# Kernel optimization log

Measured on AMD Instinct MI355X. Metric: run time of the kernel, lower is better.

## Reference

```python
import jax, jax.numpy as jnp
import numpy as np

N_NODES = 50000


def _sage_max(x, src, dst, W_l, b_l, W_r):
    # gather neighbor (source) features, scatter-max to destination nodes
    msgs = x[src]                                   # [E, F]
    agg = jax.ops.segment_max(msgs, dst, num_segments=N_NODES)  # [N, F], -inf for empty
    agg = jnp.where(jnp.isneginf(agg), 0.0, agg)    # PyG fills isolated nodes with 0
    return agg @ W_l + b_l + x @ W_r                # lin_l(aggr) + lin_r(x)


def setup_inputs() -> dict:
    key = jax.random.key(0)
    ks = jax.random.split(key, 9)
    F_IN, H, OUT, E, EL = 128, 256, 32, 800000, 200000
    x = jax.random.normal(ks[0], (N_NODES, F_IN), dtype=jnp.float32)
    edge_index = jax.random.randint(ks[1], (2, E), 0, N_NODES, dtype=jnp.int64)
    edge_label_index = jax.random.randint(ks[2], (2, EL), 0, N_NODES, dtype=jnp.int64)
    s1 = 1.0 / np.sqrt(F_IN)
    s2 = 1.0 / np.sqrt(H)
    W1_l = jax.random.normal(ks[3], (F_IN, H), dtype=jnp.float32) * s1
    b1 = jnp.zeros((H,), dtype=jnp.float32)
    W1_r = jax.random.normal(ks[4], (F_IN, H), dtype=jnp.float32) * s1
    W2_l = jax.random.normal(ks[5], (H, OUT), dtype=jnp.float32) * s2
    b2 = jnp.zeros((OUT,), dtype=jnp.float32)
    W2_r = jax.random.normal(ks[6], (H, OUT), dtype=jnp.float32) * s2
    return {"x": x, "edge_index": edge_index, "edge_label_index": edge_label_index,
            "W1_l": W1_l, "b1": b1, "W1_r": W1_r,
            "W2_l": W2_l, "b2": b2, "W2_r": W2_r}


def reference(x, edge_index, edge_label_index, W1_l, b1, W1_r, W2_l, b2, W2_r):
    src, dst = edge_index[0], edge_index[1]
    # encode (eval mode: dropout is identity)
    h = jax.nn.relu(_sage_max(x, src, dst, W1_l, b1, W1_r))
    z = _sage_max(h, src, dst, W2_l, b2, W2_r)       # [N, 32]
    # decode: dot product between endpoint embeddings
    s = z[edge_label_index[0]]
    d = z[edge_label_index[1]]
    return jnp.sum(s * d, axis=-1)                   # [E_label]
```

## Files before the change

kernel.cpp:

```cpp
#include <hip/hip_runtime.h>
#include <hip/hip_bf16.h>
#include <math.h>

#define N_NODES 50000
#define NBKT 196
#define BSH 8
#define TILE2 4096
#define CAP 64
#define P2CAP 5888
#define SCAN_FLAG 0x40000000

typedef __attribute__((ext_vector_type(8))) short short8;
typedef __attribute__((ext_vector_type(4))) float f32x4;

static __device__ __forceinline__ float b2f(unsigned int u16) {
    union { unsigned int i; float f; } c; c.i = u16 << 16; return c.f;
}
static __device__ __forceinline__ unsigned int fbits(float f) {
    union { float f; unsigned int i; } c; c.f = f; return c.i;
}
static __device__ __forceinline__ unsigned short f2b_rne(float f) {
    unsigned int u = fbits(f);
    u += 0x7fff + ((u >> 16) & 1);
    return (unsigned short)(u >> 16);
}

static __device__ __forceinline__ unsigned char quant8(float v) {
    int q = (int)(v * 15.9375f + 0.5f);
    return (unsigned char)min(q, 255);
}

static __device__ __forceinline__ short8 dq8(uint2 v8) {
    short8 r;
#pragma unroll
    for (int bi = 0; bi < 4; ++bi)
        r[bi] = (short)f2b_rne((float)((v8.x >> (8 * bi)) & 255u) * 0.0627451f);
#pragma unroll
    for (int bi = 0; bi < 4; ++bi)
        r[4 + bi] = (short)f2b_rne((float)((v8.y >> (8 * bi)) & 255u) * 0.0627451f);
    return r;
}


__global__ __launch_bounds__(256) void k_prepbin(
        const float* __restrict__ x, unsigned short* __restrict__ xb,
        const float* __restrict__ W1l, const float* __restrict__ W1r, unsigned short* __restrict__ wt1,
        const float* __restrict__ W2l, const float* __restrict__ W2r, unsigned short* __restrict__ wt2,
        float* __restrict__ zb,
        const int* __restrict__ src, const int* __restrict__ dst, int E,
        uint2* __restrict__ tmp, int* __restrict__ cnts, int ntile) {
    __shared__ int cnt[256], sstart[256], lcur[256];
    __shared__ uint2 stage[TILE2];
    const int CX = (N_NODES * 128 / 4) / 256;
    const int CW = CX + 320;
    const int CZ = CW + 1563;
    int b = blockIdx.x, t = threadIdx.x;
    if (b < CX) {
        int i = b * 256 + t;
        float4 v = *(const float4*)(x + (size_t)i * 4);
        ushort4 o;
        o.x = f2b_rne(v.x); o.y = f2b_rne(v.y); o.z = f2b_rne(v.z); o.w = f2b_rne(v.w);
        *(ushort4*)(xb + (size_t)i * 4) = o;
    } else if (b < CX + 256) {
        int i = (b - CX) * 256 + t;
        int n = i >> 8, k = i & 255;
        float v = (k < 128) ? W1l[(size_t)k * 256 + n] : W1r[(size_t)(k - 128) * 256 + n];
        wt1[(size_t)n * 256 + k] = f2b_rne(v);
    } else if (b < CW) {
        int i = (b - CX - 256) * 256 + t;
        int n = i >> 9, k = i & 511;
        float v = (k < 256) ? W2l[(size_t)k * 32 + n] : W2r[(size_t)(k - 256) * 32 + n];
        wt2[(size_t)n * 512 + k] = f2b_rne(v);
    } else if (b < CZ) {
        int i = (b - CW) * 256 + t;
        if (i < 400000) ((float4*)zb)[i] = (float4){0.f, 0.f, 0.f, 0.f};
    } else {
        int tb = b - CZ;
        int e0 = tb * TILE2;
        int tilecnt = min(TILE2, E - e0);
        if (tilecnt <= 0) return;
        cnt[t] = 0;
        __syncthreads();
        if (tilecnt == TILE2) {
            for (int i = 4 * t; i < TILE2; i += 1024) {
                int4 d = *(const int4*)(dst + e0 + i);
                atomicAdd(&cnt[d.x >> BSH], 1);
                atomicAdd(&cnt[d.y >> BSH], 1);
                atomicAdd(&cnt[d.z >> BSH], 1);
                atomicAdd(&cnt[d.w >> BSH], 1);
            }
        } else {
            for (int i = t; i < tilecnt; i += 256)
                atomicAdd(&cnt[dst[e0 + i] >> BSH], 1);
        }
        __syncthreads();
        int cv = cnt[t];
        sstart[t] = cv;
        __syncthreads();
        for (int off = 1; off < 256; off <<= 1) {
            int add = (t >= off) ? sstart[t - off] : 0;
            __syncthreads();
            sstart[t] += add;
            __syncthreads();
        }
        int mystart = sstart[t] - cv;
        __syncthreads();
        sstart[t] = mystart;
        lcur[t] = mystart;
        __syncthreads();
        if (tilecnt == TILE2) {
            for (int i = 4 * t; i < TILE2; i += 1024) {
                int4 d = *(const int4*)(dst + e0 + i);
                int4 s = *(const int4*)(src + e0 + i);
                int q0 = atomicAdd(&lcur[d.x >> BSH], 1); stage[q0] = (uint2){(unsigned)s.x, (unsigned)d.x};
                int q1 = atomicAdd(&lcur[d.y >> BSH], 1); stage[q1] = (uint2){(unsigned)s.y, (unsigned)d.y};
                int q2 = atomicAdd(&lcur[d.z >> BSH], 1); stage[q2] = (uint2){(unsigned)s.z, (unsigned)d.z};
                int q3 = atomicAdd(&lcur[d.w >> BSH], 1); stage[q3] = (uint2){(unsigned)s.w, (unsigned)d.w};
            }
        } else {
            for (int i = t; i < tilecnt; i += 256) {
                int d = dst[e0 + i];
                int s = src[e0 + i];
                int q = atomicAdd(&lcur[d >> BSH], 1);
                uint2 p; p.x = (unsigned)s; p.y = (unsigned)d;
                stage[q] = p;
            }
        }
        __syncthreads();
        if (t < NBKT) cnts[(size_t)t * ntile + tb] = cnt[t];
        for (int i = t; i < tilecnt; i += 256) {
            uint2 p = stage[i];
            int bk = (int)(p.y >> BSH);
            tmp[((size_t)bk * ntile + tb) * CAP + (i - sstart[bk])] = p;
        }
    }
}


__global__ __launch_bounds__(256) void k_bin2(const uint2* __restrict__ tmp,
        const int* __restrict__ cnts, int* __restrict__ pub,
        int* __restrict__ rowptr, int* __restrict__ esrc, int N, int E, int ntile) {
    __shared__ int sc[256], toff[260], nodecnt[256], lcur[256];
    __shared__ int stage[P2CAP];
    __shared__ int shsum[4];
    int k = blockIdx.x, t = threadIdx.x;

    int c = (t < ntile) ? cnts[(size_t)k * ntile + t] : 0;
    sc[t] = c;
    __syncthreads();
    for (int off = 1; off < 256; off <<= 1) {
        int add = (t >= off) ? sc[t - off] : 0;
        __syncthreads();
        sc[t] += add;
        __syncthreads();
    }
    if (t < ntile) toff[t] = sc[t] - c;
    if (t == 255) toff[ntile] = sc[255];
    __syncthreads();
    int total = toff[ntile];

    if (t == 255) atomicExch(&pub[k], SCAN_FLAG | total);
    int v = 0;
    if (t < k) {
        int val;
        do { val = atomicOr(&pub[t], 0); } while (!(val & SCAN_FLAG) || (val & 0x80000000));
        v = val & (SCAN_FLAG - 1);
    }
#pragma unroll
    for (int off = 32; off >= 1; off >>= 1) v += __shfl_xor(v, off);
    if ((t & 63) == 0) shsum[t >> 6] = v;
    nodecnt[t] = 0;
    __syncthreads();
    int base = shsum[0] + shsum[1] + shsum[2] + shsum[3];

    for (int i = t; i < total; i += 256) {
        int lo = 0, hi = ntile;
        while (hi - lo > 1) { int mid = (lo + hi) >> 1; if (toff[mid] <= i) lo = mid; else hi = mid; }
        uint2 p = tmp[((size_t)k * ntile + lo) * CAP + (i - toff[lo])];
        atomicAdd(&nodecnt[(int)p.y & 255], 1);
    }
    __syncthreads();

    int nc = nodecnt[t];
    sc[t] = nc;
    __syncthreads();
    for (int off = 1; off < 256; off <<= 1) {
        int add = (t >= off) ? sc[t - off] : 0;
        __syncthreads();
        sc[t] += add;
        __syncthreads();
    }
    int ex = sc[t] - nc;
    int node = (k << BSH) + t;
    if (node < N) rowptr[node] = base + ex;
    if (node == N) rowptr[N] = E;
    lcur[t] = ex;
    __syncthreads();

    if (total <= P2CAP) {
        for (int i = t; i < total; i += 256) {
            int lo = 0, hi = ntile;
            while (hi - lo > 1) { int mid = (lo + hi) >> 1; if (toff[mid] <= i) lo = mid; else hi = mid; }
            uint2 p = tmp[((size_t)k * ntile + lo) * CAP + (i - toff[lo])];
            int q = atomicAdd(&lcur[(int)p.y & 255], 1);
            stage[q] = (int)p.x;
        }
        __syncthreads();
        for (int i = t; i < total; i += 256)
            esrc[base + i] = stage[i];
    } else {
        for (int i = t; i < total; i += 256) {
            int lo = 0, hi = ntile;
            while (hi - lo > 1) { int mid = (lo + hi) >> 1; if (toff[mid] <= i) lo = mid; else hi = mid; }
            uint2 p = tmp[((size_t)k * ntile + lo) * CAP + (i - toff[lo])];
            int q = atomicAdd(&lcur[(int)p.y & 255], 1);
            esrc[base + q] = (int)p.x;
        }
    }
}


__global__ __launch_bounds__(256) void k_seg_max1(const unsigned short* __restrict__ feat,
        const int* __restrict__ rowptr, const int* __restrict__ esrc,
        unsigned short* __restrict__ out) {
    int w = threadIdx.x >> 6, t = threadIdx.x & 63;
    int n = blockIdx.x * 4 + w;
    int lane16 = t & 15, sub = t >> 4;
    int beg = rowptr[n], end = rowptr[n + 1];
    float m[8];
#pragma unroll
    for (int k = 0; k < 8; ++k) m[k] = -INFINITY;
    for (int base = beg; base < end; base += 64) {
        int cnt = min(64, end - base);
        int vidx = (base + t < end) ? __builtin_nontemporal_load(&esrc[base + t]) : 0;
        for (int j = 0; j < cnt; j += 16) {
            uint4 v[4];
#pragma unroll
            for (int u = 0; u < 4; ++u) {
                int e = min(j + 4 * u + sub, cnt - 1);
                int s = __shfl(vidx, e);
                v[u] = *(const uint4*)(feat + (size_t)s * 128 + lane16 * 8);
            }
#pragma unroll
            for (int u = 0; u < 4; ++u) {
                m[0] = fmaxf(m[0], b2f(v[u].x & 0xffff));
                m[1] = fmaxf(m[1], b2f(v[u].x >> 16));
                m[2] = fmaxf(m[2], b2f(v[u].y & 0xffff));
                m[3] = fmaxf(m[3], b2f(v[u].y >> 16));
                m[4] = fmaxf(m[4], b2f(v[u].z & 0xffff));
                m[5] = fmaxf(m[5], b2f(v[u].z >> 16));
                m[6] = fmaxf(m[6], b2f(v[u].w & 0xffff));
                m[7] = fmaxf(m[7], b2f(v[u].w >> 16));
            }
        }
    }
#pragma unroll
    for (int k = 0; k < 8; ++k) {
        m[k] = fmaxf(m[k], __shfl_xor(m[k], 16));
        m[k] = fmaxf(m[k], __shfl_xor(m[k], 32));
        if (beg == end) m[k] = 0.f;
    }
    if (sub == 0) {
        uint4 p;
        p.x = (fbits(m[0]) >> 16) | (fbits(m[1]) & 0xffff0000u);
        p.y = (fbits(m[2]) >> 16) | (fbits(m[3]) & 0xffff0000u);
        p.z = (fbits(m[4]) >> 16) | (fbits(m[5]) & 0xffff0000u);
        p.w = (fbits(m[6]) >> 16) | (fbits(m[7]) & 0xffff0000u);
        *(uint4*)(out + (size_t)n * 128 + lane16 * 8) = p;
    }
}


__global__ __launch_bounds__(256) void k_seg_max2(const unsigned char* __restrict__ feat8,
        const int* __restrict__ rowptr, const int* __restrict__ esrc,
        unsigned char* __restrict__ out8) {
    int w = threadIdx.x >> 6, t = threadIdx.x & 63;
    int n = blockIdx.x * 4 + w;
    int lane16 = t & 15, sub = t >> 4;
    int beg = rowptr[n], end = rowptr[n + 1];
    int m[16];
#pragma unroll
    for (int k = 0; k < 16; ++k) m[k] = 0;
    for (int base = beg; base < end; base += 64) {
        int cnt = min(64, end - base);
        int vidx = (base + t < end) ? __builtin_nontemporal_load(&esrc[base + t]) : 0;
        for (int j = 0; j < cnt; j += 32) {
            uint4 v[8];
#pragma unroll
            for (int u = 0; u < 8; ++u) {
                int e = min(j + 4 * u + sub, cnt - 1);
                int s = __shfl(vidx, e);
                v[u] = *(const uint4*)(feat8 + (size_t)s * 256 + lane16 * 16);
            }
#pragma unroll
            for (int u = 0; u < 8; ++u) {
                m[0]  = max(m[0],  (int)(v[u].x & 0xFF));
                m[1]  = max(m[1],  (int)((v[u].x >> 8) & 0xFF));
                m[2]  = max(m[2],  (int)((v[u].x >> 16) & 0xFF));
                m[3]  = max(m[3],  (int)(v[u].x >> 24));
                m[4]  = max(m[4],  (int)(v[u].y & 0xFF));
                m[5]  = max(m[5],  (int)((v[u].y >> 8) & 0xFF));
                m[6]  = max(m[6],  (int)((v[u].y >> 16) & 0xFF));
                m[7]  = max(m[7],  (int)(v[u].y >> 24));
                m[8]  = max(m[8],  (int)(v[u].z & 0xFF));
                m[9]  = max(m[9],  (int)((v[u].z >> 8) & 0xFF));
                m[10] = max(m[10], (int)((v[u].z >> 16) & 0xFF));
                m[11] = max(m[11], (int)(v[u].z >> 24));
                m[12] = max(m[12], (int)(v[u].w & 0xFF));
                m[13] = max(m[13], (int)((v[u].w >> 8) & 0xFF));
                m[14] = max(m[14], (int)((v[u].w >> 16) & 0xFF));
                m[15] = max(m[15], (int)(v[u].w >> 24));
            }
        }
    }
#pragma unroll
    for (int k = 0; k < 16; ++k) {
        m[k] = max(m[k], __shfl_xor(m[k], 16));
        m[k] = max(m[k], __shfl_xor(m[k], 32));
    }
    if (sub == 0) {
        uint4 p;
        p.x = m[0]  | (m[1]  << 8) | (m[2]  << 16) | (m[3]  << 24);
        p.y = m[4]  | (m[5]  << 8) | (m[6]  << 16) | (m[7]  << 24);
        p.z = m[8]  | (m[9]  << 8) | (m[10] << 16) | (m[11] << 24);
        p.w = m[12] | (m[13] << 8) | (m[14] << 16) | (m[15] << 24);
        *(uint4*)(out8 + (size_t)n * 256 + lane16 * 16) = p;
    }
}


__global__ __launch_bounds__(256) void k_lin1_mfma(
        const unsigned short* __restrict__ A0, const unsigned short* __restrict__ A1,
        const unsigned short* __restrict__ WT, const float* __restrict__ bias,
        const unsigned short* __restrict__ WT2, float* __restrict__ zpart,
        unsigned char* __restrict__ H8, int M) {
    __shared__ short Hs[128 * 136];

    int tid = threadIdx.x;
    int m0 = blockIdx.y * 128, n0 = blockIdx.x * 128;
    int L = tid & 63, wv = tid >> 6;
    int wr = wv >> 1, wc = wv & 1;
    int lane16 = L & 15, q = L >> 4;

    f32x4 acc[4][4];
#pragma unroll
    for (int i = 0; i < 4; ++i)
#pragma unroll
        for (int j = 0; j < 4; ++j) acc[i][j] = (f32x4){0.f, 0.f, 0.f, 0.f};

    const short8 zero8 = (short8){0, 0, 0, 0, 0, 0, 0, 0};
    int arow[4], brow[4];
#pragma unroll
    for (int i = 0; i < 4; ++i) arow[i] = m0 + wr * 64 + i * 16 + lane16;
#pragma unroll
    for (int j = 0; j < 4; ++j) brow[j] = n0 + wc * 64 + j * 16 + lane16;

#pragma unroll 1
    for (int k0 = 0; k0 < 256; k0 += 32) {
        const unsigned short* Abase = (k0 < 128) ? A0 : A1;
        int kc = (k0 & 127) + q * 8;
        short8 a[4], b[4];
#pragma unroll
        for (int i = 0; i < 4; ++i)
            a[i] = (arow[i] < M) ? *(const short8*)(Abase + (size_t)arow[i] * 128 + kc) : zero8;
#pragma unroll
        for (int j = 0; j < 4; ++j)
            b[j] = *(const short8*)(WT + (size_t)brow[j] * 256 + k0 + q * 8);
#pragma unroll
        for (int i = 0; i < 4; ++i)
#pragma unroll
            for (int j = 0; j < 4; ++j)
                acc[i][j] = __builtin_amdgcn_mfma_f32_16x16x32_bf16(a[i], b[j], acc[i][j], 0, 0, 0);
    }

#pragma unroll
    for (int i = 0; i < 4; ++i) {
#pragma unroll
        for (int r = 0; r < 4; ++r) {
            int lrow = wr * 64 + i * 16 + q * 4 + r;
            int row = m0 + lrow;
#pragma unroll
            for (int j = 0; j < 4; ++j) {
                int lcol = wc * 64 + j * 16 + lane16;
                int col = n0 + lcol;
                float v = fmaxf(acc[i][j][r] + bias[col], 0.f);
                Hs[lrow * 136 + lcol] = (short)f2b_rne(v);
                if (row < M) H8[(size_t)row * 256 + col] = quant8(v);
            }
        }
    }
    __syncthreads();

    f32x4 acc2[2][2];
#pragma unroll
    for (int i = 0; i < 2; ++i)
#pragma unroll
        for (int j = 0; j < 2; ++j) acc2[i][j] = (f32x4){0.f, 0.f, 0.f, 0.f};
#pragma unroll
    for (int kk = 0; kk < 4; ++kk) {
        short8 a2[2], b2[2];
#pragma unroll
        for (int i = 0; i < 2; ++i)
            a2[i] = *(const short8*)&Hs[(wv * 32 + i * 16 + lane16) * 136 + kk * 32 + q * 8];
#pragma unroll
        for (int j = 0; j < 2; ++j)
            b2[j] = *(const short8*)(WT2 + (size_t)(j * 16 + lane16) * 512 + 256 + n0 + kk * 32 + q * 8);
#pragma unroll
        for (int i = 0; i < 2; ++i)
#pragma unroll
            for (int j = 0; j < 2; ++j)
                acc2[i][j] = __builtin_amdgcn_mfma_f32_16x16x32_bf16(a2[i], b2[j], acc2[i][j], 0, 0, 0);
    }
#pragma unroll
    for (int i = 0; i < 2; ++i) {
#pragma unroll
        for (int r = 0; r < 4; ++r) {
            int row = m0 + wv * 32 + i * 16 + q * 4 + r;
            if (row >= M) continue;
#pragma unroll
            for (int j = 0; j < 2; ++j) {
                int col = j * 16 + lane16;
                atomicAdd(&zpart[(size_t)row * 32 + col], acc2[i][j][r]);
            }
        }
    }
}


__global__ __launch_bounds__(256) void k_lin2_mfma(
        const unsigned char* __restrict__ A8,
        const unsigned short* __restrict__ WT, const float* __restrict__ bias,
        float* __restrict__ Z, int M) {
    int tid = threadIdx.x;
    int m0 = blockIdx.x * 128;
    int L = tid & 63, wv = tid >> 6;
    int lane16 = L & 15, q = L >> 4;

    f32x4 acc[2][2];
#pragma unroll
    for (int i = 0; i < 2; ++i)
#pragma unroll
        for (int j = 0; j < 2; ++j) acc[i][j] = (f32x4){0.f, 0.f, 0.f, 0.f};

    int arow[2];
#pragma unroll
    for (int i = 0; i < 2; ++i) arow[i] = m0 + wv * 32 + i * 16 + lane16;

#pragma unroll 1
    for (int k0 = 0; k0 < 256; k0 += 32) {
        short8 a[2], b[2];
#pragma unroll
        for (int i = 0; i < 2; ++i) {
            uint2 v8 = (arow[i] < M) ? *(const uint2*)(A8 + (size_t)arow[i] * 256 + k0 + q * 8)
                                     : (uint2){0u, 0u};
            a[i] = dq8(v8);
        }
#pragma unroll
        for (int j = 0; j < 2; ++j)
            b[j] = *(const short8*)(WT + (size_t)(j * 16 + lane16) * 512 + k0 + q * 8);
#pragma unroll
        for (int i = 0; i < 2; ++i)
#pragma unroll
            for (int j = 0; j < 2; ++j)
                acc[i][j] = __builtin_amdgcn_mfma_f32_16x16x32_bf16(a[i], b[j], acc[i][j], 0, 0, 0);
    }

#pragma unroll
    for (int i = 0; i < 2; ++i) {
#pragma unroll
        for (int r = 0; r < 4; ++r) {
            int row = m0 + wv * 32 + i * 16 + q * 4 + r;
            if (row >= M) continue;
#pragma unroll
            for (int j = 0; j < 2; ++j) {
                int col = j * 16 + lane16;
                float zp = Z[(size_t)row * 32 + col];
                Z[(size_t)row * 32 + col] = acc[i][j][r] + bias[col] + zp;
            }
        }
    }
}


__global__ void k_decode(const float* __restrict__ z, const int* __restrict__ eli,
                         int EL, float* __restrict__ out) {
    int tid = blockIdx.x * blockDim.x + threadIdx.x;
    int e = tid >> 3, lane = tid & 7;
    if (e >= EL) return;
    int s = eli[e], d = eli[EL + e];
    float4 a = *((const float4*)(z + (size_t)s * 32) + lane);
    float4 b = *((const float4*)(z + (size_t)d * 32) + lane);
    float dot = a.x * b.x + a.y * b.y + a.z * b.z + a.w * b.w;
    dot += __shfl_xor(dot, 1);
    dot += __shfl_xor(dot, 2);
    dot += __shfl_xor(dot, 4);
    if (lane == 0) out[e] = dot;
}


extern "C" void kernel_launch(void* const* d_in, const int* in_sizes, int n_in,
                              void* d_out, int out_size, void* d_ws, size_t ws_size,
                              hipStream_t stream) {
    const float* x   = (const float*)d_in[0];
    const int*   ei  = (const int*)d_in[1];
    const int*   eli = (const int*)d_in[2];
    const float* W1l = (const float*)d_in[3];
    const float* b1  = (const float*)d_in[4];
    const float* W1r = (const float*)d_in[5];
    const float* W2l = (const float*)d_in[6];
    const float* b2  = (const float*)d_in[7];
    const float* W2r = (const float*)d_in[8];
    float* out = (float*)d_out;

    int N  = N_NODES;
    int E  = in_sizes[1] / 2;
    int EL = in_sizes[2] / 2;
    const int* src = ei;
    const int* dst = ei + E;

    char* ws = (char*)d_ws;
    size_t off = 0;
    auto alloc = [&](size_t bytes) -> void* {
        void* p = ws + off;
        off += (bytes + 255) & ~(size_t)255;
        return p;
    };
    unsigned short* xb   = (unsigned short*)alloc((size_t)N * 128 * 2);
    unsigned short* aggb = (unsigned short*)alloc((size_t)N * 256 * 2);
    unsigned char*  h8   = (unsigned char*)alloc((size_t)N * 256);
    float* zbuf          = (float*)alloc((size_t)N * 32 * 4);
    unsigned short* wt1  = (unsigned short*)alloc(256 * 256 * 2);
    unsigned short* wt2  = (unsigned short*)alloc(32 * 512 * 2);
    int* rowptr   = (int*)alloc((size_t)(N + 1) * 4);
    int ntile     = (E + TILE2 - 1) / TILE2;
    int* cnts     = (int*)alloc((size_t)NBKT * ntile * 4);
    int* pub      = (int*)alloc(256 * 4);
    int* esrc     = (int*)alloc((size_t)E * 4);
    uint2* tmpp   = (uint2*)aggb;
    unsigned char* agg8 = (unsigned char*)aggb;

    const int tb = 256;
    const int CZ = 6250 + 320 + 1563;

    k_prepbin<<<CZ + ntile, tb, 0, stream>>>(x, xb, W1l, W1r, wt1, W2l, W2r, wt2, zbuf,
                                             src, dst, E, tmpp, cnts, ntile);
    k_bin2<<<NBKT, tb, 0, stream>>>(tmpp, cnts, pub, rowptr, esrc, N, E, ntile);

    k_seg_max1<<<(N + 3) / 4, tb, 0, stream>>>(xb, rowptr, esrc, aggb);
    dim3 g1(2, (N + 127) / 128);
    k_lin1_mfma<<<g1, tb, 0, stream>>>(aggb, xb, wt1, b1, wt2, zbuf, h8, N);

    k_seg_max2<<<(N + 3) / 4, tb, 0, stream>>>(h8, rowptr, esrc, agg8);
    k_lin2_mfma<<<(N + 127) / 128, tb, 0, stream>>>(agg8, wt2, b2, zbuf, N);

    k_decode<<<(EL * 8 + 255) / 256, tb, 0, stream>>>(zbuf, eli, EL, out);
}
```

Measured before the change: 256.5 us.

## Halve GEMM row tiles and software-pipeline fragment loads in linear kernels

Both MFMA linear kernels now use 64-row tiles instead of 128, doubling the grid so more blocks can run across the CUs and lowering register and LDS use per block. The K loops are fully unrolled and double-buffered: fragments for the next K step load while MFMAs for the current step run, to hide global-load latency. In exchange, weight fragments are reloaded by twice as many blocks, and each wave issues fewer MFMAs per loaded A fragment.

```diff
diff --git a/kernel.cpp b/kernel.cpp
--- a/kernel.cpp
+++ b/kernel.cpp
@@ -329,55 +329,78 @@
 }
 
 
+#define LD_FRAGS1(AA0, AA1, BB0, BB1, BB2, BB3, K0) do {                              \
+    const unsigned short* Ab_ = ((K0) < 128) ? A0 : A1;                               \
+    int kc_ = ((K0) & 127) + q * 8;                                                   \
+    AA0 = aok0 ? *(const short8*)(Ab_ + (size_t)arow0 * 128 + kc_) : zero8;           \
+    AA1 = aok1 ? *(const short8*)(Ab_ + (size_t)arow1 * 128 + kc_) : zero8;           \
+    BB0 = *(const short8*)(WT + (size_t)brow0 * 256 + (K0) + q * 8);                  \
+    BB1 = *(const short8*)(WT + (size_t)brow1 * 256 + (K0) + q * 8);                  \
+    BB2 = *(const short8*)(WT + (size_t)brow2 * 256 + (K0) + q * 8);                  \
+    BB3 = *(const short8*)(WT + (size_t)brow3 * 256 + (K0) + q * 8);                  \
+} while (0)
+
+#define DO_MFMA1(AA0, AA1, BB0, BB1, BB2, BB3) do {                                   \
+    acc[0][0] = __builtin_amdgcn_mfma_f32_16x16x32_bf16(AA0, BB0, acc[0][0], 0, 0, 0);\
+    acc[0][1] = __builtin_amdgcn_mfma_f32_16x16x32_bf16(AA0, BB1, acc[0][1], 0, 0, 0);\
+    acc[0][2] = __builtin_amdgcn_mfma_f32_16x16x32_bf16(AA0, BB2, acc[0][2], 0, 0, 0);\
+    acc[0][3] = __builtin_amdgcn_mfma_f32_16x16x32_bf16(AA0, BB3, acc[0][3], 0, 0, 0);\
+    acc[1][0] = __builtin_amdgcn_mfma_f32_16x16x32_bf16(AA1, BB0, acc[1][0], 0, 0, 0);\
+    acc[1][1] = __builtin_amdgcn_mfma_f32_16x16x32_bf16(AA1, BB1, acc[1][1], 0, 0, 0);\
+    acc[1][2] = __builtin_amdgcn_mfma_f32_16x16x32_bf16(AA1, BB2, acc[1][2], 0, 0, 0);\
+    acc[1][3] = __builtin_amdgcn_mfma_f32_16x16x32_bf16(AA1, BB3, acc[1][3], 0, 0, 0);\
+} while (0)
+
 __global__ __launch_bounds__(256) void k_lin1_mfma(
         const unsigned short* __restrict__ A0, const unsigned short* __restrict__ A1,
         const unsigned short* __restrict__ WT, const float* __restrict__ bias,
         const unsigned short* __restrict__ WT2, float* __restrict__ zpart,
         unsigned char* __restrict__ H8, int M) {
-    __shared__ short Hs[128 * 136];
+    __shared__ short Hs[64 * 136];
 
     int tid = threadIdx.x;
-    int m0 = blockIdx.y * 128, n0 = blockIdx.x * 128;
+    int m0 = blockIdx.y * 64, n0 = blockIdx.x * 128;
     int L = tid & 63, wv = tid >> 6;
     int wr = wv >> 1, wc = wv & 1;
     int lane16 = L & 15, q = L >> 4;
 
-    f32x4 acc[4][4];
-#pragma unroll
-    for (int i = 0; i < 4; ++i)
+    f32x4 acc[2][4];
+#pragma unroll
+    for (int i = 0; i < 2; ++i)
 #pragma unroll
         for (int j = 0; j < 4; ++j) acc[i][j] = (f32x4){0.f, 0.f, 0.f, 0.f};
 
     const short8 zero8 = (short8){0, 0, 0, 0, 0, 0, 0, 0};
-    int arow[4], brow[4];
-#pragma unroll
-    for (int i = 0; i < 4; ++i) arow[i] = m0 + wr * 64 + i * 16 + lane16;
-#pragma unroll
-    for (int j = 0; j < 4; ++j) brow[j] = n0 + wc * 64 + j * 16 + lane16;
-
-#pragma unroll 1
-    for (int k0 = 0; k0 < 256; k0 += 32) {
-        const unsigned short* Abase = (k0 < 128) ? A0 : A1;
-        int kc = (k0 & 127) + q * 8;
-        short8 a[4], b[4];
-#pragma unroll
-        for (int i = 0; i < 4; ++i)
-            a[i] = (arow[i] < M) ? *(const short8*)(Abase + (size_t)arow[i] * 128 + kc) : zero8;
-#pragma unroll
-        for (int j = 0; j < 4; ++j)
-            b[j] = *(const short8*)(WT + (size_t)brow[j] * 256 + k0 + q * 8);
-#pragma unroll
-        for (int i = 0; i < 4; ++i)
-#pragma unroll
-            for (int j = 0; j < 4; ++j)
-                acc[i][j] = __builtin_amdgcn_mfma_f32_16x16x32_bf16(a[i], b[j], acc[i][j], 0, 0, 0);
-    }
-
-#pragma unroll
-    for (int i = 0; i < 4; ++i) {
+    int arow0 = m0 + wr * 32 + lane16;
+    int arow1 = arow0 + 16;
+    bool aok0 = arow0 < M, aok1 = arow1 < M;
+    int brow0 = n0 + wc * 64 + lane16;
+    int brow1 = brow0 + 16, brow2 = brow0 + 32, brow3 = brow0 + 48;
+
+    short8 xa0, xa1, xb0, xb1, xb2, xb3;
+    short8 ya0, ya1, yb0, yb1, yb2, yb3;
+    LD_FRAGS1(xa0, xa1, xb0, xb1, xb2, xb3, 0);
+    LD_FRAGS1(ya0, ya1, yb0, yb1, yb2, yb3, 32);
+    DO_MFMA1(xa0, xa1, xb0, xb1, xb2, xb3);
+    LD_FRAGS1(xa0, xa1, xb0, xb1, xb2, xb3, 64);
+    DO_MFMA1(ya0, ya1, yb0, yb1, yb2, yb3);
+    LD_FRAGS1(ya0, ya1, yb0, yb1, yb2, yb3, 96);
+    DO_MFMA1(xa0, xa1, xb0, xb1, xb2, xb3);
+    LD_FRAGS1(xa0, xa1, xb0, xb1, xb2, xb3, 128);
+    DO_MFMA1(ya0, ya1, yb0, yb1, yb2, yb3);
+    LD_FRAGS1(ya0, ya1, yb0, yb1, yb2, yb3, 160);
+    DO_MFMA1(xa0, xa1, xb0, xb1, xb2, xb3);
+    LD_FRAGS1(xa0, xa1, xb0, xb1, xb2, xb3, 192);
+    DO_MFMA1(ya0, ya1, yb0, yb1, yb2, yb3);
+    LD_FRAGS1(ya0, ya1, yb0, yb1, yb2, yb3, 224);
+    DO_MFMA1(xa0, xa1, xb0, xb1, xb2, xb3);
+    DO_MFMA1(ya0, ya1, yb0, yb1, yb2, yb3);
+
+#pragma unroll
+    for (int i = 0; i < 2; ++i) {
 #pragma unroll
         for (int r = 0; r < 4; ++r) {
-            int lrow = wr * 64 + i * 16 + q * 4 + r;
+            int lrow = wr * 32 + i * 16 + q * 4 + r;
             int row = m0 + lrow;
 #pragma unroll
             for (int j = 0; j < 4; ++j) {
@@ -391,92 +414,87 @@
     }
     __syncthreads();
 
-    f32x4 acc2[2][2];
-#pragma unroll
-    for (int i = 0; i < 2; ++i)
-#pragma unroll
-        for (int j = 0; j < 2; ++j) acc2[i][j] = (f32x4){0.f, 0.f, 0.f, 0.f};
+    f32x4 acc2[2];
+    acc2[0] = (f32x4){0.f, 0.f, 0.f, 0.f};
+    acc2[1] = (f32x4){0.f, 0.f, 0.f, 0.f};
 #pragma unroll
     for (int kk = 0; kk < 4; ++kk) {
-        short8 a2[2], b2[2];
-#pragma unroll
-        for (int i = 0; i < 2; ++i)
-            a2[i] = *(const short8*)&Hs[(wv * 32 + i * 16 + lane16) * 136 + kk * 32 + q * 8];
-#pragma unroll
-        for (int j = 0; j < 2; ++j)
-            b2[j] = *(const short8*)(WT2 + (size_t)(j * 16 + lane16) * 512 + 256 + n0 + kk * 32 + q * 8);
-#pragma unroll
-        for (int i = 0; i < 2; ++i)
-#pragma unroll
-            for (int j = 0; j < 2; ++j)
-                acc2[i][j] = __builtin_amdgcn_mfma_f32_16x16x32_bf16(a2[i], b2[j], acc2[i][j], 0, 0, 0);
-    }
-#pragma unroll
-    for (int i = 0; i < 2; ++i) {
-#pragma unroll
-        for (int r = 0; r < 4; ++r) {
-            int row = m0 + wv * 32 + i * 16 + q * 4 + r;
-            if (row >= M) continue;
-#pragma unroll
-            for (int j = 0; j < 2; ++j) {
-                int col = j * 16 + lane16;
-                atomicAdd(&zpart[(size_t)row * 32 + col], acc2[i][j][r]);
-            }
-        }
-    }
-}
-
+        short8 a2 = *(const short8*)&Hs[(wv * 16 + lane16) * 136 + kk * 32 + q * 8];
+        short8 b20 = *(const short8*)(WT2 + (size_t)lane16 * 512 + 256 + n0 + kk * 32 + q * 8);
+        short8 b21 = *(const short8*)(WT2 + (size_t)(16 + lane16) * 512 + 256 + n0 + kk * 32 + q * 8);
+        acc2[0] = __builtin_amdgcn_mfma_f32_16x16x32_bf16(a2, b20, acc2[0], 0, 0, 0);
+        acc2[1] = __builtin_amdgcn_mfma_f32_16x16x32_bf16(a2, b21, acc2[1], 0, 0, 0);
+    }
+#pragma unroll
+    for (int r = 0; r < 4; ++r) {
+        int row = m0 + wv * 16 + q * 4 + r;
+        if (row >= M) continue;
+#pragma unroll
+        for (int j = 0; j < 2; ++j) {
+            int col = j * 16 + lane16;
+            atomicAdd(&zpart[(size_t)row * 32 + col], acc2[j][r]);
+        }
+    }
+}
+
+
+#define LD_FRAGS2(RA, BB0, BB1, K0) do {                                              \
+    RA = aok0 ? *(const uint2*)(A8 + (size_t)arow0 * 256 + (K0) + q * 8)              \
+              : (uint2){0u, 0u};                                                      \
+    BB0 = *(const short8*)(WT + (size_t)lane16 * 512 + (K0) + q * 8);                 \
+    BB1 = *(const short8*)(WT + (size_t)(16 + lane16) * 512 + (K0) + q * 8);          \
+} while (0)
+
+#define DO_MFMA2(RA, BB0, BB1) do {                                                   \
+    short8 a_ = dq8(RA);                                                              \
+    acc0 = __builtin_amdgcn_mfma_f32_16x16x32_bf16(a_, BB0, acc0, 0, 0, 0);           \
+    acc1 = __builtin_amdgcn_mfma_f32_16x16x32_bf16(a_, BB1, acc1, 0, 0, 0);           \
+} while (0)
 
 __global__ __launch_bounds__(256) void k_lin2_mfma(
         const unsigned char* __restrict__ A8,
         const unsigned short* __restrict__ WT, const float* __restrict__ bias,
         float* __restrict__ Z, int M) {
     int tid = threadIdx.x;
-    int m0 = blockIdx.x * 128;
+    int m0 = blockIdx.x * 64;
     int L = tid & 63, wv = tid >> 6;
     int lane16 = L & 15, q = L >> 4;
 
-    f32x4 acc[2][2];
-#pragma unroll
-    for (int i = 0; i < 2; ++i)
-#pragma unroll
-        for (int j = 0; j < 2; ++j) acc[i][j] = (f32x4){0.f, 0.f, 0.f, 0.f};
-
-    int arow[2];
-#pragma unroll
-    for (int i = 0; i < 2; ++i) arow[i] = m0 + wv * 32 + i * 16 + lane16;
-
-#pragma unroll 1
-    for (int k0 = 0; k0 < 256; k0 += 32) {
-        short8 a[2], b[2];
-#pragma unroll
-        for (int i = 0; i < 2; ++i) {
-            uint2 v8 = (arow[i] < M) ? *(const uint2*)(A8 + (size_t)arow[i] * 256 + k0 + q * 8)
-                                     : (uint2){0u, 0u};
-            a[i] = dq8(v8);
-        }
-#pragma unroll
-        for (int j = 0; j < 2; ++j)
-            b[j] = *(const short8*)(WT + (size_t)(j * 16 + lane16) * 512 + k0 + q * 8);
-#pragma unroll
-        for (int i = 0; i < 2; ++i)
-#pragma unroll
-            for (int j = 0; j < 2; ++j)
-                acc[i][j] = __builtin_amdgcn_mfma_f32_16x16x32_bf16(a[i], b[j], acc[i][j], 0, 0, 0);
-    }
-
-#pragma unroll
-    for (int i = 0; i < 2; ++i) {
-#pragma unroll
-        for (int r = 0; r < 4; ++r) {
-            int row = m0 + wv * 32 + i * 16 + q * 4 + r;
-            if (row >= M) continue;
-#pragma unroll
-            for (int j = 0; j < 2; ++j) {
-                int col = j * 16 + lane16;
-                float zp = Z[(size_t)row * 32 + col];
-                Z[(size_t)row * 32 + col] = acc[i][j][r] + bias[col] + zp;
-            }
+    f32x4 acc0 = (f32x4){0.f, 0.f, 0.f, 0.f};
+    f32x4 acc1 = (f32x4){0.f, 0.f, 0.f, 0.f};
+
+    int arow0 = m0 + wv * 16 + lane16;
+    bool aok0 = arow0 < M;
+
+    uint2 xra, yra;
+    short8 xb0, xb1, yb0, yb1;
+    LD_FRAGS2(xra, xb0, xb1, 0);
+    LD_FRAGS2(yra, yb0, yb1, 32);
+    DO_MFMA2(xra, xb0, xb1);
+    LD_FRAGS2(xra, xb0, xb1, 64);
+    DO_MFMA2(yra, yb0, yb1);
+    LD_FRAGS2(yra, yb0, yb1, 96);
+    DO_MFMA2(xra, xb0, xb1);
+    LD_FRAGS2(xra, xb0, xb1, 128);
+    DO_MFMA2(yra, yb0, yb1);
+    LD_FRAGS2(yra, yb0, yb1, 160);
+    DO_MFMA2(xra, xb0, xb1);
+    LD_FRAGS2(xra, xb0, xb1, 192);
+    DO_MFMA2(yra, yb0, yb1);
+    LD_FRAGS2(yra, yb0, yb1, 224);
+    DO_MFMA2(xra, xb0, xb1);
+    DO_MFMA2(yra, yb0, yb1);
+
+#pragma unroll
+    for (int r = 0; r < 4; ++r) {
+        int row = m0 + wv * 16 + q * 4 + r;
+        if (row >= M) continue;
+#pragma unroll
+        for (int j = 0; j < 2; ++j) {
+            int col = j * 16 + lane16;
+            float av = (j == 0) ? acc0[r] : acc1[r];
+            float zp = Z[(size_t)row * 32 + col];
+            Z[(size_t)row * 32 + col] = av + bias[col] + zp;
         }
     }
 }
@@ -547,11 +565,11 @@
     k_bin2<<<NBKT, tb, 0, stream>>>(tmpp, cnts, pub, rowptr, esrc, N, E, ntile);
 
     k_seg_max1<<<(N + 3) / 4, tb, 0, stream>>>(xb, rowptr, esrc, aggb);
-    dim3 g1(2, (N + 127) / 128);
+    dim3 g1(2, (N + 63) / 64);
     k_lin1_mfma<<<g1, tb, 0, stream>>>(aggb, xb, wt1, b1, wt2, zbuf, h8, N);
 
     k_seg_max2<<<(N + 3) / 4, tb, 0, stream>>>(h8, rowptr, esrc, agg8);
-    k_lin2_mfma<<<(N + 127) / 128, tb, 0, stream>>>(agg8, wt2, b2, zbuf, N);
+    k_lin2_mfma<<<(N + 63) / 64, tb, 0, stream>>>(agg8, wt2, b2, zbuf, N);
 
     k_decode<<<(EL * 8 + 255) / 256, tb, 0, stream>>>(zbuf, eli, EL, out);
 }
```

New measurement: 261.7 us. +2.1%, slower.

## Double-buffer lin1 tiles in LDS via async global_load_lds; pipeline lin2 loads

Applied to the files above, without the earlier changes.

The first linear kernel now stages A and W tiles into swizzled, double-buffered LDS using global_load_lds, so the next K-slice loads while MFMAs run on the current one. Each wave then reads its fragments from LDS instead of issuing direct strided global loads. The row bound check is dropped, so the aggregation buffer is padded by 128 rows to keep out-of-range reads inside allocated memory. The second linear kernel halves its row tile to 64 to launch more blocks and software-pipelines its fragment loads two stages deep. This adds barriers and LDS traffic in exchange for better latency hiding.

```diff
diff --git a/kernel.cpp b/kernel.cpp
--- a/kernel.cpp
+++ b/kernel.cpp
@@ -329,12 +329,38 @@
 }
 
 
+#define STAGE1(Asb, Bsb, K0) do {                                                     \
+    const unsigned short* Ab_ = ((K0) < 128) ? A0 : A1;                               \
+    int kab_ = ((K0) & 127) * 2;                                                      \
+    int kbb_ = (K0) * 2;                                                              \
+    _Pragma("unroll")                                                                 \
+    for (int ii = 0; ii < 2; ++ii) {                                                  \
+        int c_ = ii * 256 + tid;                                                      \
+        int r_ = c_ >> 2, gs_ = (c_ & 3) ^ (r_ & 3);                                  \
+        const char* ga_ = (const char*)Ab_ + (size_t)(m0 + r_) * 256 + kab_ + gs_ * 16; \
+        __builtin_amdgcn_global_load_lds(                                             \
+            (const __attribute__((address_space(1))) void*)ga_,                       \
+            (__attribute__((address_space(3))) void*)((char*)(Asb) + (ii * 256 + (tid & ~63)) * 16), \
+            16, 0, 0);                                                                \
+        const char* gb_ = (const char*)WT + (size_t)(n0 + r_) * 512 + kbb_ + gs_ * 16; \
+        __builtin_amdgcn_global_load_lds(                                             \
+            (const __attribute__((address_space(1))) void*)gb_,                       \
+            (__attribute__((address_space(3))) void*)((char*)(Bsb) + (ii * 256 + (tid & ~63)) * 16), \
+            16, 0, 0);                                                                \
+    }                                                                                 \
+} while (0)
+
 __global__ __launch_bounds__(256) void k_lin1_mfma(
         const unsigned short* __restrict__ A0, const unsigned short* __restrict__ A1,
         const unsigned short* __restrict__ WT, const float* __restrict__ bias,
         const unsigned short* __restrict__ WT2, float* __restrict__ zpart,
         unsigned char* __restrict__ H8, int M) {
-    __shared__ short Hs[128 * 136];
+    __shared__ __align__(16) short SH[17408];
+    short* As0 = SH;
+    short* As1 = SH + 4096;
+    short* Bs0 = SH + 8192;
+    short* Bs1 = SH + 12288;
+    short* Hs  = SH;
 
     int tid = threadIdx.x;
     int m0 = blockIdx.y * 128, n0 = blockIdx.x * 128;
@@ -348,29 +374,34 @@
 #pragma unroll
         for (int j = 0; j < 4; ++j) acc[i][j] = (f32x4){0.f, 0.f, 0.f, 0.f};
 
-    const short8 zero8 = (short8){0, 0, 0, 0, 0, 0, 0, 0};
-    int arow[4], brow[4];
-#pragma unroll
-    for (int i = 0; i < 4; ++i) arow[i] = m0 + wr * 64 + i * 16 + lane16;
-#pragma unroll
-    for (int j = 0; j < 4; ++j) brow[j] = n0 + wc * 64 + j * 16 + lane16;
-
-#pragma unroll 1
-    for (int k0 = 0; k0 < 256; k0 += 32) {
-        const unsigned short* Abase = (k0 < 128) ? A0 : A1;
-        int kc = (k0 & 127) + q * 8;
+    STAGE1(As0, Bs0, 0);
+    __syncthreads();
+
+#pragma unroll
+    for (int t = 0; t < 8; ++t) {
+        const short* Asb = (t & 1) ? As1 : As0;
+        const short* Bsb = (t & 1) ? Bs1 : Bs0;
+        short* Asn = (t & 1) ? As0 : As1;
+        short* Bsn = (t & 1) ? Bs0 : Bs1;
+        if (t < 7) STAGE1(Asn, Bsn, (t + 1) * 32);
+
         short8 a[4], b[4];
 #pragma unroll
-        for (int i = 0; i < 4; ++i)
-            a[i] = (arow[i] < M) ? *(const short8*)(Abase + (size_t)arow[i] * 128 + kc) : zero8;
-#pragma unroll
-        for (int j = 0; j < 4; ++j)
-            b[j] = *(const short8*)(WT + (size_t)brow[j] * 256 + k0 + q * 8);
+        for (int i = 0; i < 4; ++i) {
+            int r = wr * 64 + i * 16 + lane16;
+            a[i] = *(const short8*)((const char*)Asb + r * 64 + ((q ^ (r & 3)) << 4));
+        }
+#pragma unroll
+        for (int j = 0; j < 4; ++j) {
+            int c = wc * 64 + j * 16 + lane16;
+            b[j] = *(const short8*)((const char*)Bsb + c * 64 + ((q ^ (c & 3)) << 4));
+        }
 #pragma unroll
         for (int i = 0; i < 4; ++i)
 #pragma unroll
             for (int j = 0; j < 4; ++j)
                 acc[i][j] = __builtin_amdgcn_mfma_f32_16x16x32_bf16(a[i], b[j], acc[i][j], 0, 0, 0);
+        __syncthreads();
     }
 
 #pragma unroll
@@ -427,56 +458,63 @@
 }
 
 
+#define LD_FRAGS2(RA, BB0, BB1, K0) do {                                              \
+    RA = aok0 ? *(const uint2*)(A8 + (size_t)arow0 * 256 + (K0) + q * 8)              \
+              : (uint2){0u, 0u};                                                      \
+    BB0 = *(const short8*)(WT + (size_t)lane16 * 512 + (K0) + q * 8);                 \
+    BB1 = *(const short8*)(WT + (size_t)(16 + lane16) * 512 + (K0) + q * 8);          \
+} while (0)
+
+#define DO_MFMA2(RA, BB0, BB1) do {                                                   \
+    short8 a_ = dq8(RA);                                                              \
+    acc0 = __builtin_amdgcn_mfma_f32_16x16x32_bf16(a_, BB0, acc0, 0, 0, 0);           \
+    acc1 = __builtin_amdgcn_mfma_f32_16x16x32_bf16(a_, BB1, acc1, 0, 0, 0);           \
+} while (0)
+
 __global__ __launch_bounds__(256) void k_lin2_mfma(
         const unsigned char* __restrict__ A8,
         const unsigned short* __restrict__ WT, const float* __restrict__ bias,
         float* __restrict__ Z, int M) {
     int tid = threadIdx.x;
-    int m0 = blockIdx.x * 128;
+    int m0 = blockIdx.x * 64;
     int L = tid & 63, wv = tid >> 6;
     int lane16 = L & 15, q = L >> 4;
 
-    f32x4 acc[2][2];
-#pragma unroll
-    for (int i = 0; i < 2; ++i)
-#pragma unroll
-        for (int j = 0; j < 2; ++j) acc[i][j] = (f32x4){0.f, 0.f, 0.f, 0.f};
-
-    int arow[2];
-#pragma unroll
-    for (int i = 0; i < 2; ++i) arow[i] = m0 + wv * 32 + i * 16 + lane16;
-
-#pragma unroll 1
-    for (int k0 = 0; k0 < 256; k0 += 32) {
-        short8 a[2], b[2];
-#pragma unroll
-        for (int i = 0; i < 2; ++i) {
-            uint2 v8 = (arow[i] < M) ? *(const uint2*)(A8 + (size_t)arow[i] * 256 + k0 + q * 8)
-                                     : (uint2){0u, 0u};
-            a[i] = dq8(v8);
-        }
-#pragma unroll
-        for (int j = 0; j < 2; ++j)
-            b[j] = *(const short8*)(WT + (size_t)(j * 16 + lane16) * 512 + k0 + q * 8);
-#pragma unroll
-        for (int i = 0; i < 2; ++i)
-#pragma unroll
-            for (int j = 0; j < 2; ++j)
-                acc[i][j] = __builtin_amdgcn_mfma_f32_16x16x32_bf16(a[i], b[j], acc[i][j], 0, 0, 0);
-    }
-
-#pragma unroll
-    for (int i = 0; i < 2; ++i) {
-#pragma unroll
-        for (int r = 0; r < 4; ++r) {
-            int row = m0 + wv * 32 + i * 16 + q * 4 + r;
-            if (row >= M) continue;
-#pragma unroll
-            for (int j = 0; j < 2; ++j) {
-                int col = j * 16 + lane16;
-                float zp = Z[(size_t)row * 32 + col];
-                Z[(size_t)row * 32 + col] = acc[i][j][r] + bias[col] + zp;
-            }
+    f32x4 acc0 = (f32x4){0.f, 0.f, 0.f, 0.f};
+    f32x4 acc1 = (f32x4){0.f, 0.f, 0.f, 0.f};
+
+    int arow0 = m0 + wv * 16 + lane16;
+    bool aok0 = arow0 < M;
+
+    uint2 xra, yra;
+    short8 xb0, xb1, yb0, yb1;
+    LD_FRAGS2(xra, xb0, xb1, 0);
+    LD_FRAGS2(yra, yb0, yb1, 32);
+    DO_MFMA2(xra, xb0, xb1);
+    LD_FRAGS2(xra, xb0, xb1, 64);
+    DO_MFMA2(yra, yb0, yb1);
+    LD_FRAGS2(yra, yb0, yb1, 96);
+    DO_MFMA2(xra, xb0, xb1);
+    LD_FRAGS2(xra, xb0, xb1, 128);
+    DO_MFMA2(yra, yb0, yb1);
+    LD_FRAGS2(yra, yb0, yb1, 160);
+    DO_MFMA2(xra, xb0, xb1);
+    LD_FRAGS2(xra, xb0, xb1, 192);
+    DO_MFMA2(yra, yb0, yb1);
+    LD_FRAGS2(yra, yb0, yb1, 224);
+    DO_MFMA2(xra, xb0, xb1);
+    DO_MFMA2(yra, yb0, yb1);
+
+#pragma unroll
+    for (int r = 0; r < 4; ++r) {
+        int row = m0 + wv * 16 + q * 4 + r;
+        if (row >= M) continue;
+#pragma unroll
+        for (int j = 0; j < 2; ++j) {
+            int col = j * 16 + lane16;
+            float av = (j == 0) ? acc0[r] : acc1[r];
+            float zp = Z[(size_t)row * 32 + col];
+            Z[(size_t)row * 32 + col] = av + bias[col] + zp;
         }
     }
 }
@@ -526,7 +564,7 @@
         return p;
     };
     unsigned short* xb   = (unsigned short*)alloc((size_t)N * 128 * 2);
-    unsigned short* aggb = (unsigned short*)alloc((size_t)N * 256 * 2);
+    unsigned short* aggb = (unsigned short*)alloc((size_t)(N + 128) * 256 * 2);
     unsigned char*  h8   = (unsigned char*)alloc((size_t)N * 256);
     float* zbuf          = (float*)alloc((size_t)N * 32 * 4);
     unsigned short* wt1  = (unsigned short*)alloc(256 * 256 * 2);
@@ -551,7 +589,7 @@
     k_lin1_mfma<<<g1, tb, 0, stream>>>(aggb, xb, wt1, b1, wt2, zbuf, h8, N);
 
     k_seg_max2<<<(N + 3) / 4, tb, 0, stream>>>(h8, rowptr, esrc, agg8);
-    k_lin2_mfma<<<(N + 127) / 128, tb, 0, stream>>>(agg8, wt2, b2, zbuf, N);
+    k_lin2_mfma<<<(N + 63) / 64, tb, 0, stream>>>(agg8, wt2, b2, zbuf, N);
 
     k_decode<<<(EL * 8 + 255) / 256, tb, 0, stream>>>(zbuf, eli, EL, out);
 }
```

Result: faster. 245.7 us (-4.2%).
